# Kernel tuning notes

Hardware: AMD Instinct MI355X
Metric: run time of the kernel (lower is better)

Reference implementation:

```python
import jax, jax.numpy as jnp
import numpy as np

EMBED_DIM = 1024
NUM_HEADS = 16
HEAD_DIM = EMBED_DIM // NUM_HEADS
RANK = 512
B, S = 4, 4096


def setup_inputs() -> dict:
    key = jax.random.key(0)
    ks = jax.random.split(key, 16)
    sd = 0.02
    inp = {
        "query": jax.random.normal(ks[0], (B, S, EMBED_DIM), jnp.float32),
        "key": jax.random.normal(ks[1], (B, S, EMBED_DIM), jnp.float32),
        "value": jax.random.normal(ks[2], (B, S, EMBED_DIM), jnp.float32),
        # torch nn.Linear weights: [out_features, in_features]
        "q_down_w": jax.random.normal(ks[3], (RANK, EMBED_DIM), jnp.float32) * sd,
        "q_up_w": jax.random.normal(ks[4], (EMBED_DIM, RANK), jnp.float32) * sd,
        "q_up_b": jax.random.normal(ks[5], (EMBED_DIM,), jnp.float32) * sd,
        "k_down_w": jax.random.normal(ks[6], (RANK, EMBED_DIM), jnp.float32) * sd,
        "k_up_w": jax.random.normal(ks[7], (EMBED_DIM, RANK), jnp.float32) * sd,
        "k_up_b": jax.random.normal(ks[8], (EMBED_DIM,), jnp.float32) * sd,
        "v_down_w": jax.random.normal(ks[9], (RANK, EMBED_DIM), jnp.float32) * sd,
        "v_up_w": jax.random.normal(ks[10], (EMBED_DIM, RANK), jnp.float32) * sd,
        "v_up_b": jax.random.normal(ks[11], (EMBED_DIM,), jnp.float32) * sd,
        "out_w": jax.random.normal(ks[12], (EMBED_DIM, EMBED_DIM), jnp.float32) * sd,
        "out_b": jax.random.normal(ks[13], (EMBED_DIM,), jnp.float32) * sd,
    }
    return inp


def _linear(x, w, b=None):
    y = x @ w.T
    return y if b is None else y + b


def reference(query, key, value,
              q_down_w, q_up_w, q_up_b,
              k_down_w, k_up_w, k_up_b,
              v_down_w, v_up_w, v_up_b,
              out_w, out_b):
    b, s, _ = query.shape
    # low-rank QKV projections
    q = _linear(_linear(query, q_down_w), q_up_w, q_up_b)
    k = _linear(_linear(key, k_down_w), k_up_w, k_up_b)
    v = _linear(_linear(value, v_down_w), v_up_w, v_up_b)
    # [B,S,E] -> [B,H,S,Dh]
    q = q.reshape(b, s, NUM_HEADS, HEAD_DIM).transpose(0, 2, 1, 3)
    k = k.reshape(b, s, NUM_HEADS, HEAD_DIM).transpose(0, 2, 1, 3)
    v = v.reshape(b, s, NUM_HEADS, HEAD_DIM).transpose(0, 2, 1, 3)
    # kernel feature map: elu + 1  (note: scaling_factor in original is computed but unused)
    q = jax.nn.elu(q) + 1.0
    k = jax.nn.elu(k) + 1.0
    k_sum = k.sum(axis=-2)                              # [B,H,Dh]
    denom = jnp.einsum('bhnd,bhd->bhn', q, k_sum)       # [B,H,S]
    kv = jnp.einsum('bhnd,bhne->bhde', k, v)            # [B,H,Dh,Dh]
    num = jnp.einsum('bhnd,bhde->bhne', q, kv)          # [B,H,S,Dh]
    out = num / (denom[..., None] + 1e-6)
    out = out.transpose(0, 2, 1, 3).reshape(b, s, EMBED_DIM)
    return _linear(out, out_w, out_b)
```

## Files before the change

### kernel.cpp

```cpp
#include <hip/hip_runtime.h>
#include <hip/hip_bf16.h>

typedef unsigned short ushort_t;
typedef unsigned int uint_t;
typedef __attribute__((ext_vector_type(8))) short short8;
typedef __attribute__((ext_vector_type(4))) float f32x4;

#define EMBED 1024
#define RANK  512
#define BB    4
#define SS    4096
#define HH    16
#define DHD   64
#define MM    (BB*SS)
#define NCHUNK 16

__device__ __forceinline__ float bf2f(ushort_t u) {
    union { uint_t i; float f; } v; v.i = ((uint_t)u) << 16; return v.f;
}
__device__ __forceinline__ ushort_t f2bf(float f) {
    union { float f; uint_t i; } v; v.f = f;
    uint_t r = v.i + 0x7FFFu + ((v.i >> 16) & 1u);
    return (ushort_t)(r >> 16);
}
__device__ __forceinline__ void gl2lds16(const void* g, void* l) {
    __builtin_amdgcn_global_load_lds((const __attribute__((address_space(1))) void*)g,
                                     (__attribute__((address_space(3))) void*)l,
                                     16, 0, 0);
}

template<int EPI>
__global__ __launch_bounds__(256) void gemm_bt(
    const ushort_t* __restrict__ A0, const ushort_t* __restrict__ A1, const ushort_t* __restrict__ A2,
    const ushort_t* __restrict__ B0, const ushort_t* __restrict__ B1, const ushort_t* __restrict__ B2,
    const float* __restrict__ bias0, const float* __restrict__ bias1, const float* __restrict__ bias2,
    void* __restrict__ C0, void* __restrict__ C1, void* __restrict__ C2,
    int N, int K, int nbx)
{
    __shared__ __align__(16) char lds_raw[49152];

    const int z = blockIdx.z;
    const ushort_t* Ab   = (z == 0) ? A0 : (z == 1) ? A1 : A2;
    const ushort_t* Bm   = (z == 0) ? B0 : (z == 1) ? B1 : B2;
    const float*    bias = (z == 0) ? bias0 : (z == 1) ? bias1 : bias2;
    void*           Cv   = (z == 0) ? C0 : (z == 1) ? C1 : C2;

    const int cpx = gridDim.x >> 3;
    const int bid = blockIdx.x;
    const int wg  = (bid & 7) * cpx + (bid >> 3);
    const long m0 = (long)(wg / nbx) * 128;
    const long n0 = (long)(wg % nbx) * 128;

    const int t = threadIdx.x;
    const int lane = t & 63;
    const int w = t >> 6;
    const int wr = (w >> 1) * 64;
    const int wc = (w & 1) * 64;
    const int fr = lane & 15;
    const int kq = (lane >> 4) * 8;

    const int srow = t >> 2;
    const int scol = ((t & 3) ^ ((srow >> 1) & 3)) * 8;
    const int kqs = (((kq >> 3) ^ ((fr >> 1) & 3))) * 8;

    auto STAGE = [&](int k0, int buf) {
        char* Ad = lds_raw + buf * 8192;
        char* Bd = lds_raw + 24576 + buf * 8192;
        #pragma unroll
        for (int ro = 0; ro < 2; ++ro) {
            const int row = ro * 64 + srow;
            gl2lds16(Ab + (m0 + row) * (long)K + k0 + scol, Ad + (ro * 256 + w * 64) * 16);
            gl2lds16(Bm + (n0 + row) * (long)K + k0 + scol, Bd + (ro * 256 + w * 64) * 16);
        }
    };

    f32x4 acc[4][4] = {};
    const int nt = K >> 5;

    STAGE(0, 0);
    STAGE(32, 1);

    int cur = 0;
    for (int ti = 0; ti < nt; ++ti) {
        if (ti + 1 < nt) { asm volatile("s_waitcnt vmcnt(4)" ::: "memory"); }
        else             { asm volatile("s_waitcnt vmcnt(0)" ::: "memory"); }
        __builtin_amdgcn_sched_barrier(0);
        __builtin_amdgcn_s_barrier();
        __builtin_amdgcn_sched_barrier(0);

        int nb = cur + 2; if (nb >= 3) nb -= 3;
        if (ti + 2 < nt) STAGE((ti + 2) << 5, nb);

        const ushort_t* Asc = (const ushort_t*)(lds_raw + cur * 8192);
        const ushort_t* Bsc = (const ushort_t*)(lds_raw + 24576 + cur * 8192);
        short8 av[4], bv[4];
        #pragma unroll
        for (int mi = 0; mi < 4; ++mi)
            av[mi] = *(const short8*)&Asc[(wr + mi * 16 + fr) * 32 + kqs];
        #pragma unroll
        for (int nf = 0; nf < 4; ++nf)
            bv[nf] = *(const short8*)&Bsc[(wc + nf * 16 + fr) * 32 + kqs];
        #pragma unroll
        for (int mi = 0; mi < 4; ++mi)
            #pragma unroll
            for (int nf = 0; nf < 4; ++nf)
                acc[mi][nf] = __builtin_amdgcn_mfma_f32_16x16x32_bf16(
                    av[mi], bv[nf], acc[mi][nf], 0, 0, 0);

        ++cur; if (cur == 3) cur = 0;
    }

    const int rj = (lane >> 4) * 4;
    if (EPI == 3) {
        float* Cf = (float*)Cv;
        __syncthreads();
        #pragma unroll
        for (int nf = 0; nf < 4; ++nf) {
            const long col = n0 + wc + nf * 16 + fr;
            const float bval = bias[col];
            #pragma unroll
            for (int mi = 0; mi < 4; ++mi)
                #pragma unroll
                for (int j = 0; j < 4; ++j)
                    Cf[(m0 + wr + mi * 16 + rj + j) * (long)N + col] = acc[mi][nf][j] + bval;
        }
    } else {
        ushort_t* Ct = (ushort_t*)lds_raw;
        __syncthreads();
        const bool do_elu = (EPI == 2) && (z < 2);
        #pragma unroll
        for (int nf = 0; nf < 4; ++nf) {
            const int coll = wc + nf * 16 + fr;
            const float bval = (EPI >= 2) ? bias[n0 + coll] : 0.0f;
            #pragma unroll
            for (int mi = 0; mi < 4; ++mi) {
                #pragma unroll
                for (int j = 0; j < 4; ++j) {
                    float x = acc[mi][nf][j];
                    if (EPI >= 2) x += bval;
                    if (do_elu) x = (x > 0.0f) ? (x + 1.0f) : __expf(x);
                    Ct[(wr + mi * 16 + rj + j) * 136 + coll] = f2bf(x);
                }
            }
        }
        __syncthreads();
        ushort_t* Cb = (ushort_t*)Cv;
        #pragma unroll
        for (int it = 0; it < 8; ++it) {
            const int idx = it * 256 + t;
            const int r   = idx >> 4;
            const int c8  = (idx & 15) * 8;
            short8 vv = *(const short8*)&Ct[r * 136 + c8];
            *(short8*)(Cb + (m0 + r) * (long)N + n0 + c8) = vv;
        }
    }
}

__global__ __launch_bounds__(256) void gemm_dn(
    const float* __restrict__ A0, const float* __restrict__ A1, const float* __restrict__ A2,
    const ushort_t* __restrict__ B0, const ushort_t* __restrict__ B1, const ushort_t* __restrict__ B2,
    void* __restrict__ C0, void* __restrict__ C1, void* __restrict__ C2,
    int N, int K, int nbx)
{
    __shared__ __align__(16) char lds_raw[36864];

    const int z = blockIdx.z;
    const float*    Af = (z == 0) ? A0 : (z == 1) ? A1 : A2;
    const ushort_t* Bm = (z == 0) ? B0 : (z == 1) ? B1 : B2;
    void*           Cv = (z == 0) ? C0 : (z == 1) ? C1 : C2;

    const int cpx = gridDim.x >> 3;
    const int bid = blockIdx.x;
    const int wg  = (bid & 7) * cpx + (bid >> 3);
    const long m0 = (long)(wg / nbx) * 128;
    const long n0 = (long)(wg % nbx) * 128;

    const int t = threadIdx.x;
    const int lane = t & 63;
    const int w = t >> 6;
    const int wr = (w >> 1) * 64;
    const int wc = (w & 1) * 64;
    const int fr = lane & 15;
    const int kq = (lane >> 4) * 8;

    const int srow = t >> 2;
    const int scol = ((t & 3) ^ ((srow >> 1) & 3)) * 8;
    const int kqs = (((kq >> 3) ^ ((fr >> 1) & 3))) * 8;

    const int arow  = t >> 1;
    const int acolh = (t & 1) * 16;
    const int asw   = (arow >> 1) & 3;
    const int as0   = (2 * (t & 1)) ^ asw;
    const int as1   = (2 * (t & 1) + 1) ^ asw;

    auto LOADA = [&](int k0, f32x4* ra) {
        const float* src = Af + (m0 + arow) * (long)K + k0 + acolh;
        #pragma unroll
        for (int j = 0; j < 4; ++j) ra[j] = *(const f32x4*)(src + 4 * j);
    };
    auto LOADB = [&](int k0, int buf) {
        char* Bd = lds_raw + 16384 + buf * 8192;
        #pragma unroll
        for (int ro = 0; ro < 2; ++ro) {
            const int row = ro * 64 + srow;
            gl2lds16(Bm + (n0 + row) * (long)K + k0 + scol, Bd + (ro * 256 + w * 64) * 16);
        }
    };
    auto WRITEA = [&](const f32x4* ra, int buf) {
        ushort_t* Ad = (ushort_t*)(lds_raw + buf * 8192);
        short8 h0, h1;
        #pragma unroll
        for (int j = 0; j < 4; ++j) {
            h0[2 * j]     = (short)f2bf(ra[j >> 1][(j & 1) * 2]);
            h0[2 * j + 1] = (short)f2bf(ra[j >> 1][(j & 1) * 2 + 1]);
            h1[2 * j]     = (short)f2bf(ra[2 + (j >> 1)][(j & 1) * 2]);
            h1[2 * j + 1] = (short)f2bf(ra[2 + (j >> 1)][(j & 1) * 2 + 1]);
        }
        *(short8*)&Ad[arow * 32 + as0 * 8] = h0;
        *(short8*)&Ad[arow * 32 + as1 * 8] = h1;
    };

    f32x4 acc[4][4] = {};
    const int nt = K >> 5;

    f32x4 ra[4];
    LOADA(0, ra);
    LOADB(0, 0);
    WRITEA(ra, 0);
    __syncthreads();

    int cur = 0;
    for (int ti = 0; ti < nt; ++ti) {
        if (ti + 1 < nt) {
            LOADA((ti + 1) << 5, ra);
            LOADB((ti + 1) << 5, cur ^ 1);
        }

        const ushort_t* Asc = (const ushort_t*)(lds_raw + cur * 8192);
        const ushort_t* Bsc = (const ushort_t*)(lds_raw + 16384 + cur * 8192);
        short8 av[4], bv[4];
        #pragma unroll
        for (int mi = 0; mi < 4; ++mi)
            av[mi] = *(const short8*)&Asc[(wr + mi * 16 + fr) * 32 + kqs];
        #pragma unroll
        for (int nf = 0; nf < 4; ++nf)
            bv[nf] = *(const short8*)&Bsc[(wc + nf * 16 + fr) * 32 + kqs];
        #pragma unroll
        for (int mi = 0; mi < 4; ++mi)
            #pragma unroll
            for (int nf = 0; nf < 4; ++nf)
                acc[mi][nf] = __builtin_amdgcn_mfma_f32_16x16x32_bf16(
                    av[mi], bv[nf], acc[mi][nf], 0, 0, 0);

        if (ti + 1 < nt) WRITEA(ra, cur ^ 1);
        __syncthreads();
        cur ^= 1;
    }

    ushort_t* Ct = (ushort_t*)lds_raw;
    const int rj = (lane >> 4) * 4;
    #pragma unroll
    for (int nf = 0; nf < 4; ++nf) {
        const int coll = wc + nf * 16 + fr;
        #pragma unroll
        for (int mi = 0; mi < 4; ++mi)
            #pragma unroll
            for (int j = 0; j < 4; ++j)
                Ct[(wr + mi * 16 + rj + j) * 136 + coll] = f2bf(acc[mi][nf][j]);
    }
    __syncthreads();
    ushort_t* Cb = (ushort_t*)Cv;
    #pragma unroll
    for (int it = 0; it < 8; ++it) {
        const int idx = it * 256 + t;
        const int r   = idx >> 4;
        const int c8  = (idx & 15) * 8;
        short8 vv = *(const short8*)&Ct[r * 136 + c8];
        *(short8*)(Cb + (m0 + r) * (long)N + n0 + c8) = vv;
    }
}

__global__ __launch_bounds__(256) void cvt_weights(
    const float* __restrict__ s0, const float* __restrict__ s1,
    const float* __restrict__ s2, const float* __restrict__ s3,
    const float* __restrict__ s4, const float* __restrict__ s5,
    const float* __restrict__ s6,
    ushort_t* __restrict__ d0, ushort_t* __restrict__ d1,
    ushort_t* __restrict__ d2, ushort_t* __restrict__ d3,
    ushort_t* __restrict__ d4, ushort_t* __restrict__ d5,
    ushort_t* __restrict__ d6)
{
    const int y = blockIdx.y;
    const float* src; ushort_t* dst; int n;
    switch (y) {
        case 0: src = s0; dst = d0; n = RANK * EMBED; break;
        case 1: src = s1; dst = d1; n = RANK * EMBED; break;
        case 2: src = s2; dst = d2; n = RANK * EMBED; break;
        case 3: src = s3; dst = d3; n = RANK * EMBED; break;
        case 4: src = s4; dst = d4; n = RANK * EMBED; break;
        case 5: src = s5; dst = d5; n = RANK * EMBED; break;
        default: src = s6; dst = d6; n = EMBED * EMBED; break;
    }
    const int i = (blockIdx.x * 256 + threadIdx.x) * 4;
    if (i < n) {
        f32x4 f = *(const f32x4*)(src + i);
        typedef __attribute__((ext_vector_type(4))) short short4v;
        short4v h;
        h[0] = (short)f2bf(f[0]); h[1] = (short)f2bf(f[1]);
        h[2] = (short)f2bf(f[2]); h[3] = (short)f2bf(f[3]);
        *(short4v*)(dst + i) = h;
    }
}

__global__ __launch_bounds__(256) void kv_stats(const ushort_t* __restrict__ Kp,
                                                const ushort_t* __restrict__ Vp,
                                                float* __restrict__ kvp,
                                                float* __restrict__ ksump)
{
    __shared__ __align__(16) ushort_t Ks[64 * 64];
    __shared__ __align__(16) ushort_t Vs[64 * 64];
    const int t = threadIdx.x;
    const int w = t >> 6;
    const int bh = blockIdx.x;
    const int chunk = blockIdx.y;
    const int b = bh >> 4, h = bh & 15;
    const int d0 = (t & 15) * 4;
    const int e0 = (t >> 4) * 4;
    float acc[4][4] = {};
    float sks[4] = {};
    const long hbase = ((long)b * SS) * EMBED + h * DHD;

    for (int sub = 0; sub < 4; ++sub) {
        const int n00 = chunk * 256 + sub * 64;
        #pragma unroll
        for (int ro = 0; ro < 2; ++ro) {
            const int idx = ro * 256 + t;
            const int r = idx >> 3, c16 = idx & 7;
            const long g = hbase + (long)(n00 + r) * EMBED + c16 * 8;
            gl2lds16(Kp + g, (char*)Ks + (ro * 256 + w * 64) * 16);
            gl2lds16(Vp + g, (char*)Vs + (ro * 256 + w * 64) * 16);
        }
        __syncthreads();
        #pragma unroll 8
        for (int n = 0; n < 64; ++n) {
            const uint_t* kr = (const uint_t*)(Ks + n * 64 + d0);
            const uint_t* vr = (const uint_t*)(Vs + n * 64 + e0);
            const uint_t k01 = kr[0], k23 = kr[1];
            const uint_t v01 = vr[0], v23 = vr[1];
            float kd[4], ve[4];
            {
                union { uint_t i; float f; } a, bq, c, dq;
                a.i = k01 << 16; bq.i = k01 & 0xffff0000u;
                c.i = k23 << 16; dq.i = k23 & 0xffff0000u;
                kd[0] = a.f; kd[1] = bq.f; kd[2] = c.f; kd[3] = dq.f;
            }
            {
                union { uint_t i; float f; } a, bq, c, dq;
                a.i = v01 << 16; bq.i = v01 & 0xffff0000u;
                c.i = v23 << 16; dq.i = v23 & 0xffff0000u;
                ve[0] = a.f; ve[1] = bq.f; ve[2] = c.f; ve[3] = dq.f;
            }
            #pragma unroll
            for (int e = 0; e < 4; ++e)
                #pragma unroll
                for (int d = 0; d < 4; ++d)
                    acc[e][d] += ve[e] * kd[d];
            if (e0 == 0) {
                #pragma unroll
                for (int d = 0; d < 4; ++d) sks[d] += kd[d];
            }
        }
        __syncthreads();
    }

    float* dst = kvp + ((long)chunk * 64 + bh) * 4096;
    #pragma unroll
    for (int e = 0; e < 4; ++e) {
        f32x4 vv; vv[0] = acc[e][0]; vv[1] = acc[e][1]; vv[2] = acc[e][2]; vv[3] = acc[e][3];
        *(f32x4*)(dst + (e0 + e) * 64 + d0) = vv;
    }
    if (e0 == 0) {
        float* sd = ksump + ((long)chunk * 64 + bh) * 64 + d0;
        #pragma unroll
        for (int d = 0; d < 4; ++d) sd[d] = sks[d];
    }
}

__global__ __launch_bounds__(256) void kv_reduce(const float* __restrict__ kvp,
                                                 const float* __restrict__ ksump,
                                                 ushort_t* __restrict__ kvb,
                                                 float* __restrict__ ksumf)
{
    const int bh = blockIdx.x;
    const int t = threadIdx.x;
    const long base = (long)bh * 4096 + t * 16;
    f32x4 s[4] = {};
    #pragma unroll 4
    for (int c = 0; c < NCHUNK; ++c) {
        const float* src = kvp + (long)c * 64 * 4096 + base;
        #pragma unroll
        for (int j = 0; j < 4; ++j) s[j] += *(const f32x4*)(src + j * 4);
    }
    short8 o0, o1;
    #pragma unroll
    for (int j = 0; j < 4; ++j) {
        o0[j]     = (short)f2bf(s[0][j]); o0[4 + j] = (short)f2bf(s[1][j]);
        o1[j]     = (short)f2bf(s[2][j]); o1[4 + j] = (short)f2bf(s[3][j]);
    }
    *(short8*)(kvb + base)     = o0;
    *(short8*)(kvb + base + 8) = o1;

    if (t < 64) {
        float ss = 0.f;
        #pragma unroll
        for (int c = 0; c < NCHUNK; ++c) ss += ksump[(long)c * 64 * 64 + bh * 64 + t];
        ksumf[bh * 64 + t] = ss;
    }
}

__global__ __launch_bounds__(256) void attn_out(const ushort_t* __restrict__ Qp,
                                                const ushort_t* __restrict__ kvb,
                                                const float* __restrict__ ksum,
                                                ushort_t* __restrict__ Op)
{
    __shared__ __align__(16) ushort_t Qs[128 * 64];
    __shared__ __align__(16) ushort_t KVs[64 * 64];
    __shared__ float kss[64];
    __shared__ float dnm[128];
    const int t = threadIdx.x;
    const int w = t >> 6, lane = t & 63;
    const int bh = blockIdx.x, mc = blockIdx.y;
    const int b = bh >> 4, h = bh & 15;
    const long base = ((long)b * SS + mc * 128) * EMBED + h * DHD;

    #pragma unroll
    for (int ro = 0; ro < 4; ++ro) {
        const int idx = ro * 256 + t;
        const int r = idx >> 3, c16 = idx & 7;
        gl2lds16(Qp + base + (long)r * EMBED + c16 * 8,
                 (char*)Qs + (ro * 256 + w * 64) * 16);
    }
    #pragma unroll
    for (int ro = 0; ro < 2; ++ro) {
        const int idx = ro * 256 + t;
        gl2lds16(kvb + (long)bh * 4096 + idx * 8,
                 (char*)KVs + (ro * 256 + w * 64) * 16);
    }
    if (t < 64) kss[t] = ksum[bh * 64 + t];
    __syncthreads();

    if (t < 128) {
        float s = 0.f;
        const uint_t* qr = (const uint_t*)(Qs + t * 64);
        #pragma unroll
        for (int jj = 0; jj < 32; ++jj) {
            const uint_t u = qr[jj];
            union { uint_t i; float f; } lo, hi;
            lo.i = u << 16; hi.i = u & 0xffff0000u;
            s += lo.f * kss[2 * jj] + hi.f * kss[2 * jj + 1];
        }
        dnm[t] = s;
    }

    const int fr = lane & 15, kq = (lane >> 4) * 8;
    f32x4 acc[2][4] = {};
    #pragma unroll
    for (int ks = 0; ks < 2; ++ks) {
        short8 av[2], bv[4];
        #pragma unroll
        for (int mi = 0; mi < 2; ++mi)
            av[mi] = *(const short8*)&Qs[(w * 32 + mi * 16 + fr) * 64 + ks * 32 + kq];
        #pragma unroll
        for (int nf = 0; nf < 4; ++nf)
            bv[nf] = *(const short8*)&KVs[(nf * 16 + fr) * 64 + ks * 32 + kq];
        #pragma unroll
        for (int mi = 0; mi < 2; ++mi)
            #pragma unroll
            for (int nf = 0; nf < 4; ++nf)
                acc[mi][nf] = __builtin_amdgcn_mfma_f32_16x16x32_bf16(
                    av[mi], bv[nf], acc[mi][nf], 0, 0, 0);
    }
    __syncthreads();

    const int rj = (lane >> 4) * 4;
    #pragma unroll
    for (int mi = 0; mi < 2; ++mi) {
        #pragma unroll
        for (int nf = 0; nf < 4; ++nf) {
            #pragma unroll
            for (int j = 0; j < 4; ++j) {
                const int r = w * 32 + mi * 16 + rj + j;
                const int c = nf * 16 + fr;
                const float x = acc[mi][nf][j] / (dnm[r] + 1e-6f);
                Op[base + (long)r * EMBED + c] = f2bf(x);
            }
        }
    }
}

extern "C" void kernel_launch(void* const* d_in, const int* in_sizes, int n_in,
                              void* d_out, int out_size, void* d_ws, size_t ws_size,
                              hipStream_t stream)
{
    (void)in_sizes; (void)n_in; (void)out_size; (void)ws_size;
    const float* query = (const float*)d_in[0];
    const float* key_  = (const float*)d_in[1];
    const float* value = (const float*)d_in[2];
    const float* q_dw  = (const float*)d_in[3];
    const float* q_uw  = (const float*)d_in[4];
    const float* q_ub  = (const float*)d_in[5];
    const float* k_dw  = (const float*)d_in[6];
    const float* k_uw  = (const float*)d_in[7];
    const float* k_ub  = (const float*)d_in[8];
    const float* v_dw  = (const float*)d_in[9];
    const float* v_uw  = (const float*)d_in[10];
    const float* v_ub  = (const float*)d_in[11];
    const float* o_w   = (const float*)d_in[12];
    const float* o_b   = (const float*)d_in[13];

    char* ws = (char*)d_ws;
    size_t off = 0;
    auto alloc = [&](size_t bytes) -> void* {
        void* p = ws + off;
        off += (bytes + 255) & ~(size_t)255;
        return p;
    };
    const size_t WSMALL = (size_t)RANK * EMBED;
    ushort_t* bw_qd = (ushort_t*)alloc(WSMALL * 2);
    ushort_t* bw_qu = (ushort_t*)alloc(WSMALL * 2);
    ushort_t* bw_kd = (ushort_t*)alloc(WSMALL * 2);
    ushort_t* bw_ku = (ushort_t*)alloc(WSMALL * 2);
    ushort_t* bw_vd = (ushort_t*)alloc(WSMALL * 2);
    ushort_t* bw_vu = (ushort_t*)alloc(WSMALL * 2);
    ushort_t* bw_o  = (ushort_t*)alloc((size_t)EMBED * EMBED * 2);
    ushort_t* PQ    = (ushort_t*)alloc((size_t)MM * EMBED * 2);
    ushort_t* PK    = (ushort_t*)alloc((size_t)MM * EMBED * 2);
    ushort_t* PV    = (ushort_t*)alloc((size_t)MM * EMBED * 2);
    ushort_t* Y1q   = (ushort_t*)alloc((size_t)MM * RANK * 2);
    ushort_t* Y1k   = (ushort_t*)alloc((size_t)MM * RANK * 2);
    ushort_t* Y1v   = (ushort_t*)alloc((size_t)MM * RANK * 2);
    float*    ksump = (float*)alloc((size_t)NCHUNK * 64 * 64 * 4);
    float*    ksumf = (float*)alloc((size_t)64 * 64 * 4);
    ushort_t* kvb   = (ushort_t*)alloc((size_t)64 * 64 * 64 * 2);

    float*    kvp = (float*)Y1q;
    ushort_t* O   = Y1k;

    const dim3 blk(256);

    cvt_weights<<<dim3(EMBED * EMBED / 1024, 7), blk, 0, stream>>>(
        q_dw, q_uw, k_dw, k_uw, v_dw, v_uw, o_w,
        bw_qd, bw_qu, bw_kd, bw_ku, bw_vd, bw_vu, bw_o);

    gemm_dn<<<dim3(MM / 128 * (RANK / 128), 1, 3), blk, 0, stream>>>(
        query, key_, value,
        bw_qd, bw_kd, bw_vd,
        Y1q, Y1k, Y1v,
        RANK, EMBED, RANK / 128);

    gemm_bt<2><<<dim3(MM / 128 * (EMBED / 128), 1, 3), blk, 0, stream>>>(
        Y1q, Y1k, Y1v,
        bw_qu, bw_ku, bw_vu,
        q_ub, k_ub, v_ub,
        PQ, PK, PV,
        EMBED, RANK, EMBED / 128);

    kv_stats<<<dim3(64, NCHUNK), blk, 0, stream>>>(PK, PV, kvp, ksump);
    kv_reduce<<<dim3(64), blk, 0, stream>>>(kvp, ksump, kvb, ksumf);
    attn_out<<<dim3(64, 32), blk, 0, stream>>>(PQ, kvb, ksumf, O);

    gemm_bt<3><<<dim3(MM / 128 * (EMBED / 128), 1, 1), blk, 0, stream>>>(
        O, nullptr, nullptr,
        bw_o, nullptr, nullptr,
        o_b, nullptr, nullptr,
        d_out, nullptr, nullptr,
        EMBED, EMBED, EMBED / 128);
}
```

Measured before the change: 318.5 us.

## Stream fp32 A tiles via LDS DMA with triple buffering; pack kv_stats math

The down-projection GEMM now copies the fp32 activation tile straight into LDS with global_load_lds instead of going through registers, using a swizzled layout and a three-stage buffer ring. A single barrier per iteration, guarded by a partial vmcnt wait, replaces the register-staged double buffer. Conversion to bf16 moves to fragment-load time using v_cvt_pk_bf16_f32. This doubles the LDS footprint, which may lower occupancy, and repeats the conversion for each wave that reads the same data. kv_stats switches to two-wide float vectors so the compiler can emit packed FMAs.

```diff
diff --git a/kernel.cpp b/kernel.cpp
--- a/kernel.cpp
+++ b/kernel.cpp
@@ -5,6 +5,7 @@
 typedef unsigned int uint_t;
 typedef __attribute__((ext_vector_type(8))) short short8;
 typedef __attribute__((ext_vector_type(4))) float f32x4;
+typedef __attribute__((ext_vector_type(2))) float f32x2;
 
 #define EMBED 1024
 #define RANK  512
@@ -18,10 +19,18 @@
 __device__ __forceinline__ float bf2f(ushort_t u) {
     union { uint_t i; float f; } v; v.i = ((uint_t)u) << 16; return v.f;
 }
+__device__ __forceinline__ float asf(uint_t u) {
+    union { uint_t i; float f; } v; v.i = u; return v.f;
+}
 __device__ __forceinline__ ushort_t f2bf(float f) {
     union { float f; uint_t i; } v; v.f = f;
     uint_t r = v.i + 0x7FFFu + ((v.i >> 16) & 1u);
     return (ushort_t)(r >> 16);
+}
+__device__ __forceinline__ uint_t cvtpk(float lo, float hi) {
+    uint_t r;
+    asm("v_cvt_pk_bf16_f32 %0, %1, %2" : "=v"(r) : "v"(lo), "v"(hi));
+    return r;
 }
 __device__ __forceinline__ void gl2lds16(const void* g, void* l) {
     __builtin_amdgcn_global_load_lds((const __attribute__((address_space(1))) void*)g,
@@ -162,7 +171,7 @@
     void* __restrict__ C0, void* __restrict__ C1, void* __restrict__ C2,
     int N, int K, int nbx)
 {
-    __shared__ __align__(16) char lds_raw[36864];
+    __shared__ __align__(16) char lds_raw[73728];
 
     const int z = blockIdx.z;
     const float*    Af = (z == 0) ? A0 : (z == 1) ? A1 : A2;
@@ -181,67 +190,64 @@
     const int wr = (w >> 1) * 64;
     const int wc = (w & 1) * 64;
     const int fr = lane & 15;
-    const int kq = (lane >> 4) * 8;
+    const int kq4 = lane >> 4;
+    const int fx  = fr & 7;
 
     const int srow = t >> 2;
     const int scol = ((t & 3) ^ ((srow >> 1) & 3)) * 8;
-    const int kqs = (((kq >> 3) ^ ((fr >> 1) & 3))) * 8;
-
-    const int arow  = t >> 1;
-    const int acolh = (t & 1) * 16;
-    const int asw   = (arow >> 1) & 3;
-    const int as0   = (2 * (t & 1)) ^ asw;
-    const int as1   = (2 * (t & 1) + 1) ^ asw;
-
-    auto LOADA = [&](int k0, f32x4* ra) {
-        const float* src = Af + (m0 + arow) * (long)K + k0 + acolh;
-        #pragma unroll
-        for (int j = 0; j < 4; ++j) ra[j] = *(const f32x4*)(src + 4 * j);
-    };
-    auto LOADB = [&](int k0, int buf) {
-        char* Bd = lds_raw + 16384 + buf * 8192;
-        #pragma unroll
-        for (int ro = 0; ro < 2; ++ro) {
-            const int row = ro * 64 + srow;
-            gl2lds16(Bm + (n0 + row) * (long)K + k0 + scol, Bd + (ro * 256 + w * 64) * 16);
-        }
-    };
-    auto WRITEA = [&](const f32x4* ra, int buf) {
-        ushort_t* Ad = (ushort_t*)(lds_raw + buf * 8192);
-        short8 h0, h1;
-        #pragma unroll
-        for (int j = 0; j < 4; ++j) {
-            h0[2 * j]     = (short)f2bf(ra[j >> 1][(j & 1) * 2]);
-            h0[2 * j + 1] = (short)f2bf(ra[j >> 1][(j & 1) * 2 + 1]);
-            h1[2 * j]     = (short)f2bf(ra[2 + (j >> 1)][(j & 1) * 2]);
-            h1[2 * j + 1] = (short)f2bf(ra[2 + (j >> 1)][(j & 1) * 2 + 1]);
-        }
-        *(short8*)&Ad[arow * 32 + as0 * 8] = h0;
-        *(short8*)&Ad[arow * 32 + as1 * 8] = h1;
+    const int kqs = ((kq4 ^ ((fr >> 1) & 3))) * 8;
+
+    const int sArow = t >> 3;
+    const int sAcol = ((t & 7) ^ (sArow & 7)) * 4;
+
+    auto STAGE = [&](int k0, int buf) {
+        char* Ad = lds_raw + buf * 16384;
+        char* Bd = lds_raw + 49152 + buf * 8192;
+        #pragma unroll
+        for (int p = 0; p < 4; ++p)
+            gl2lds16(Af + (m0 + p * 32 + sArow) * (long)K + k0 + sAcol,
+                     Ad + p * 4096 + w * 1024);
+        #pragma unroll
+        for (int ro = 0; ro < 2; ++ro)
+            gl2lds16(Bm + (n0 + ro * 64 + srow) * (long)K + k0 + scol,
+                     Bd + (ro * 256 + w * 64) * 16);
     };
 
     f32x4 acc[4][4] = {};
     const int nt = K >> 5;
 
-    f32x4 ra[4];
-    LOADA(0, ra);
-    LOADB(0, 0);
-    WRITEA(ra, 0);
-    __syncthreads();
+    STAGE(0, 0);
+    STAGE(32, 1);
 
     int cur = 0;
     for (int ti = 0; ti < nt; ++ti) {
-        if (ti + 1 < nt) {
-            LOADA((ti + 1) << 5, ra);
-            LOADB((ti + 1) << 5, cur ^ 1);
-        }
-
-        const ushort_t* Asc = (const ushort_t*)(lds_raw + cur * 8192);
-        const ushort_t* Bsc = (const ushort_t*)(lds_raw + 16384 + cur * 8192);
+        if (ti + 1 < nt) { asm volatile("s_waitcnt vmcnt(6)" ::: "memory"); }
+        else             { asm volatile("s_waitcnt vmcnt(0)" ::: "memory"); }
+        __builtin_amdgcn_sched_barrier(0);
+        __builtin_amdgcn_s_barrier();
+        __builtin_amdgcn_sched_barrier(0);
+
+        int nb = cur + 2; if (nb >= 3) nb -= 3;
+        if (ti + 2 < nt) STAGE((ti + 2) << 5, nb);
+
+        const float*    Asf = (const float*)(lds_raw + cur * 16384);
+        const ushort_t* Bsc = (const ushort_t*)(lds_raw + 49152 + cur * 8192);
+
         short8 av[4], bv[4];
         #pragma unroll
-        for (int mi = 0; mi < 4; ++mi)
-            av[mi] = *(const short8*)&Asc[(wr + mi * 16 + fr) * 32 + kqs];
+        for (int mi = 0; mi < 4; ++mi) {
+            const int rowoff = (wr + mi * 16 + fr) * 32;
+            const int s0 = (2 * kq4) ^ fx;
+            const int s1 = (2 * kq4 + 1) ^ fx;
+            f32x4 a0 = *(const f32x4*)&Asf[rowoff + s0 * 4];
+            f32x4 a1 = *(const f32x4*)&Asf[rowoff + s1 * 4];
+            union { uint_t u[4]; short8 s; } pk;
+            pk.u[0] = cvtpk(a0[0], a0[1]);
+            pk.u[1] = cvtpk(a0[2], a0[3]);
+            pk.u[2] = cvtpk(a1[0], a1[1]);
+            pk.u[3] = cvtpk(a1[2], a1[3]);
+            av[mi] = pk.s;
+        }
         #pragma unroll
         for (int nf = 0; nf < 4; ++nf)
             bv[nf] = *(const short8*)&Bsc[(wc + nf * 16 + fr) * 32 + kqs];
@@ -252,13 +258,12 @@
                 acc[mi][nf] = __builtin_amdgcn_mfma_f32_16x16x32_bf16(
                     av[mi], bv[nf], acc[mi][nf], 0, 0, 0);
 
-        if (ti + 1 < nt) WRITEA(ra, cur ^ 1);
-        __syncthreads();
-        cur ^= 1;
-    }
-
+        ++cur; if (cur == 3) cur = 0;
+    }
+
+    const int rj = kq4 * 4;
     ushort_t* Ct = (ushort_t*)lds_raw;
-    const int rj = (lane >> 4) * 4;
+    __syncthreads();
     #pragma unroll
     for (int nf = 0; nf < 4; ++nf) {
         const int coll = wc + nf * 16 + fr;
@@ -326,8 +331,8 @@
     const int b = bh >> 4, h = bh & 15;
     const int d0 = (t & 15) * 4;
     const int e0 = (t >> 4) * 4;
-    float acc[4][4] = {};
-    float sks[4] = {};
+    f32x2 acc2[4][2] = {};
+    f32x2 sks2[2] = {};
     const long hbase = ((long)b * SS) * EMBED + h * DHD;
 
     for (int sub = 0; sub < 4; ++sub) {
@@ -347,28 +352,19 @@
             const uint_t* vr = (const uint_t*)(Vs + n * 64 + e0);
             const uint_t k01 = kr[0], k23 = kr[1];
             const uint_t v01 = vr[0], v23 = vr[1];
-            float kd[4], ve[4];
-            {
-                union { uint_t i; float f; } a, bq, c, dq;
-                a.i = k01 << 16; bq.i = k01 & 0xffff0000u;
-                c.i = k23 << 16; dq.i = k23 & 0xffff0000u;
-                kd[0] = a.f; kd[1] = bq.f; kd[2] = c.f; kd[3] = dq.f;
+            f32x2 kd0, kd1;
+            kd0[0] = asf(k01 << 16); kd0[1] = asf(k01 & 0xffff0000u);
+            kd1[0] = asf(k23 << 16); kd1[1] = asf(k23 & 0xffff0000u);
+            float ve[4];
+            ve[0] = asf(v01 << 16); ve[1] = asf(v01 & 0xffff0000u);
+            ve[2] = asf(v23 << 16); ve[3] = asf(v23 & 0xffff0000u);
+            #pragma unroll
+            for (int e = 0; e < 4; ++e) {
+                f32x2 vb; vb[0] = ve[e]; vb[1] = ve[e];
+                acc2[e][0] += vb * kd0;
+                acc2[e][1] += vb * kd1;
             }
-            {
-                union { uint_t i; float f; } a, bq, c, dq;
-                a.i = v01 << 16; bq.i = v01 & 0xffff0000u;
-                c.i = v23 << 16; dq.i = v23 & 0xffff0000u;
-                ve[0] = a.f; ve[1] = bq.f; ve[2] = c.f; ve[3] = dq.f;
-            }
-            #pragma unroll
-            for (int e = 0; e < 4; ++e)
-                #pragma unroll
-                for (int d = 0; d < 4; ++d)
-                    acc[e][d] += ve[e] * kd[d];
-            if (e0 == 0) {
-                #pragma unroll
-                for (int d = 0; d < 4; ++d) sks[d] += kd[d];
-            }
+            if (e0 == 0) { sks2[0] += kd0; sks2[1] += kd1; }
         }
         __syncthreads();
     }
@@ -376,13 +372,15 @@
     float* dst = kvp + ((long)chunk * 64 + bh) * 4096;
     #pragma unroll
     for (int e = 0; e < 4; ++e) {
-        f32x4 vv; vv[0] = acc[e][0]; vv[1] = acc[e][1]; vv[2] = acc[e][2]; vv[3] = acc[e][3];
+        f32x4 vv;
+        vv[0] = acc2[e][0][0]; vv[1] = acc2[e][0][1];
+        vv[2] = acc2[e][1][0]; vv[3] = acc2[e][1][1];
         *(f32x4*)(dst + (e0 + e) * 64 + d0) = vv;
     }
     if (e0 == 0) {
         float* sd = ksump + ((long)chunk * 64 + bh) * 64 + d0;
-        #pragma unroll
-        for (int d = 0; d < 4; ++d) sd[d] = sks[d];
+        sd[0] = sks2[0][0]; sd[1] = sks2[0][1];
+        sd[2] = sks2[1][0]; sd[3] = sks2[1][1];
     }
 }
 
```

New measurement: 302.3 us. 1.05x faster.
